# Performance work log

Measured on AMD Instinct MI355X. Metric: run time of the kernel, lower is better.

Reference implementation:

```python
import jax, jax.numpy as jnp
import numpy as np

H = 2048  # hidden_dim


def setup_inputs() -> dict:
    key = jax.random.key(0)
    ks = jax.random.split(key, 7)
    s = 1.0 / np.sqrt(H)
    x = jax.random.normal(ks[0], (4, 2048, H), dtype=jnp.float32)
    Wq = jax.random.uniform(ks[1], (H, H), jnp.float32, -s, s)
    Wk = jax.random.uniform(ks[2], (H, H), jnp.float32, -s, s)
    Wv = jax.random.uniform(ks[3], (H, H), jnp.float32, -s, s)
    Wo = jax.random.uniform(ks[4], (H, H), jnp.float32, -s, s)
    W1 = jax.random.uniform(ks[5], (H, H), jnp.float32, -s, s)
    W2 = jax.random.uniform(ks[6], (H, H), jnp.float32, -s, s)
    return {"x": x, "Wq": Wq, "Wk": Wk, "Wv": Wv, "Wo": Wo, "W1": W1, "W2": W2}


def reference(x, Wq, Wk, Wv, Wo, W1, W2):
    # Attention (single head, no 1/sqrt(d) scaling, no mask "" faithful to source)
    q = jnp.einsum('bsh,dh->bsd', x, Wq)
    k = jnp.einsum('bsh,dh->bsd', x, Wk)
    v = jnp.einsum('bsh,dh->bsd', x, Wv)
    score = jax.nn.softmax(jnp.einsum('bqd,bkd->bqk', q, k), axis=-1)
    attn = jnp.einsum('bqk,bkd->bqd', score, v)
    attn = jnp.einsum('bsh,dh->bsd', attn, Wo)
    # FFN
    h = jax.nn.relu(jnp.einsum('bsh,dh->bsd', attn, W1))
    y = jnp.einsum('bsh,dh->bsd', h, W2)
    return jnp.sum(y)
```

## Files before the change

kernel.cpp:

```cpp
#include <hip/hip_runtime.h>
#include <hip/hip_bf16.h>
#include <stdint.h>

typedef _Float16 h16_t;
typedef __attribute__((ext_vector_type(8))) _Float16 h16x8;
typedef __attribute__((ext_vector_type(4))) _Float16 h16x4;
typedef __attribute__((ext_vector_type(16))) float f32x16;

static constexpr int HDIM  = 2048;
static constexpr int MROWS = 8192;

__device__ __forceinline__ void gload_lds16(const h16_t* g, h16_t* l) {
  __builtin_amdgcn_global_load_lds(
      (const __attribute__((address_space(1))) void*)g,
      (__attribute__((address_space(3))) void*)l, 16, 0, 0);
}

__device__ __forceinline__ uint32_t ldsaddr(const void* p) {
  return (uint32_t)(uintptr_t)(const __attribute__((address_space(3))) void*)p;
}

__device__ __forceinline__ h16x8 dsread(uint32_t off) {
  h16x8 r;
  asm volatile("ds_read_b128 %0, %1" : "=v"(r) : "v"(off));
  return r;
}

__device__ __forceinline__ void sbar()  { __builtin_amdgcn_sched_barrier(0); }
__device__ __forceinline__ void bar()   { sbar(); __builtin_amdgcn_s_barrier(); sbar(); }
__device__ __forceinline__ void waitlg0(){ asm volatile("s_waitcnt lgkmcnt(0)" ::: "memory"); sbar(); }
__device__ __forceinline__ void waitvm4(){ asm volatile("s_waitcnt vmcnt(4)" ::: "memory"); sbar(); }
__device__ __forceinline__ void waitvm0(){ asm volatile("s_waitcnt vmcnt(0)" ::: "memory"); sbar(); }

__device__ __forceinline__ void gemm_core(const h16_t* __restrict__ A,
                                          const h16_t* __restrict__ B,
                                          f32x16 acc[2][2],
                                          h16_t* sA, h16_t* sB) {
  const int tid  = threadIdx.x;
  const int wid  = tid >> 6;
  const int lane = tid & 63;
  const int wr  = (wid >> 1) << 6;
  const int wc  = (wid & 1) << 6;
  const int l31 = lane & 31;
  const int hi  = lane >> 5;
  const int sx  = lane & 7;

#pragma unroll
  for (int i = 0; i < 2; i++)
#pragma unroll
    for (int j = 0; j < 2; j++)
#pragma unroll
      for (int r = 0; r < 16; r++) acc[i][j][r] = 0.0f;

  for (int k0 = 0; k0 < 2048; k0 += 64) {
    __syncthreads();
#pragma unroll
    for (int rnd = 0; rnd < 4; rnd++) {
      const int cid  = rnd * 256 + tid;
      const int row  = cid >> 3;
      const int koct = (cid & 7) ^ (row & 7);
      const long long goff = (long long)row * 2048 + k0 + koct * 8;
      gload_lds16(A + goff, sA + (rnd * 256 + wid * 64) * 8);
      gload_lds16(B + goff, sB + (rnd * 256 + wid * 64) * 8);
    }
    __syncthreads();

#pragma unroll
    for (int ko = 0; ko < 4; ko++) {
      const int po = (2 * ko + hi) ^ sx;
      h16x8 fa[2], fb[2];
#pragma unroll
      for (int i = 0; i < 2; i++)
        fa[i] = *(const h16x8*)(sA + (wr + i * 32 + l31) * 64 + po * 8);
#pragma unroll
      for (int j = 0; j < 2; j++)
        fb[j] = *(const h16x8*)(sB + (wc + j * 32 + l31) * 64 + po * 8);
#pragma unroll
      for (int i = 0; i < 2; i++)
#pragma unroll
        for (int j = 0; j < 2; j++)
          acc[i][j] = __builtin_amdgcn_mfma_f32_32x32x16_f16(
              fa[i], fb[j], acc[i][j], 0, 0, 0);
    }
  }
}

__device__ __forceinline__ void store_c(h16_t* __restrict__ C,
                                        f32x16 acc[2][2], int bm, int bn) {
  const int tid  = threadIdx.x;
  const int wid  = tid >> 6;
  const int lane = tid & 63;
  const int wr = (wid >> 1) << 6, wc = (wid & 1) << 6;
  const int l31 = lane & 31, hi = lane >> 5;
  const int gr = bm * 128 + wr + 4 * hi;
  const int gc = bn * 128 + wc + l31;
#pragma unroll
  for (int i = 0; i < 2; i++)
#pragma unroll
    for (int r = 0; r < 16; r++) {
      const int row = gr + i * 32 + (r & 3) + 8 * (r >> 2);
      const long long ro = (long long)row * 2048;
#pragma unroll
      for (int j = 0; j < 2; j++)
        C[ro + gc + j * 32] = (h16_t)acc[i][j][r];
    }
}

__global__ __launch_bounds__(256)
void gemm_b(const h16_t* __restrict__ Ab, const h16_t* __restrict__ Bb,
            h16_t* __restrict__ Cb, long long sAz, long long sBz, long long sCz)
{
  __shared__ __align__(16) h16_t sA[128 * 64];
  __shared__ __align__(16) h16_t sB[128 * 64];
  const int bn = blockIdx.x, bm = blockIdx.y, z = blockIdx.z;
  const h16_t* A = Ab + (long long)z * sAz + (long long)bm * 128 * 2048;
  const h16_t* B = Bb + (long long)z * sBz + (long long)bn * 128 * 2048;
  f32x16 acc[2][2];
  gemm_core(A, B, acc, sA, sB);
  store_c(Cb + (long long)z * sCz, acc, bm, bn);
}

__device__ __forceinline__ void core256(const h16_t* __restrict__ A,
                                        const h16_t* __restrict__ B,
                                        h16_t* smem, f32x16 acc[4][2])
{
  const int tid  = threadIdx.x;
  const int wid  = tid >> 6, lane = tid & 63;
  const int wr2  = wid >> 2, wcid = wid & 3;
  const int l31  = lane & 31, hi = lane >> 5, sx = lane & 7;

  h16_t* pA[2] = { smem,          smem + 32768 };
  h16_t* pB[2] = { smem + 16384,  smem + 49152 };

  uint32_t poB[4];
#pragma unroll
  for (int ks = 0; ks < 4; ks++) poB[ks] = (uint32_t)((((2 * ks + hi) ^ sx) << 4));
  const uint32_t lrow = (uint32_t)(l31 * 128);
  const uint32_t aT0 = ldsaddr(pA[0]) + (uint32_t)(wr2 * 16384) + lrow;
  const uint32_t aT1 = ldsaddr(pA[1]) + (uint32_t)(wr2 * 16384) + lrow;
  const uint32_t bT0 = ldsaddr(pB[0]) + (uint32_t)(wcid * 8192) + lrow;
  const uint32_t bT1 = ldsaddr(pB[1]) + (uint32_t)(wcid * 8192) + lrow;

  const int srow = tid >> 3;
  const long long stOff = (long long)srow * HDIM + (long long)(((tid & 7) ^ (srow & 7)) * 8);
  const int dOff = tid * 8;

  auto stage1 = [&](const h16_t* M, h16_t* panel, int k0, int ci) {
    gload_lds16(M + stOff + k0 + (long long)ci * (64 * HDIM),
                panel + ci * 4096 + dOff);
  };

#pragma unroll
  for (int i = 0; i < 4; i++)
#pragma unroll
    for (int j = 0; j < 2; j++)
#pragma unroll
      for (int r = 0; r < 16; r++) acc[i][j][r] = 0.0f;

  h16x8 fA[2][4], fB0[4], fB1[4];

  auto rdA = [&](uint32_t base) {
#pragma unroll
    for (int mi = 0; mi < 2; mi++)
#pragma unroll
      for (int ks = 0; ks < 4; ks++)
        fA[mi][ks] = dsread(base + (uint32_t)(mi * 4096) + poB[ks]);
  };
  auto rdB = [&](h16x8 (&fb)[4], uint32_t base) {
#pragma unroll
    for (int ks = 0; ks < 4; ks++) fb[ks] = dsread(base + poB[ks]);
  };
  auto mm8 = [&](int am0, int nj, h16x8 (&fb)[4]) {
#pragma unroll
    for (int ks = 0; ks < 4; ks++)
#pragma unroll
      for (int mi = 0; mi < 2; mi++)
        acc[am0 + mi][nj] = __builtin_amdgcn_mfma_f32_32x32x16_f16(
            fA[mi][ks], fb[ks], acc[am0 + mi][nj], 0, 0, 0);
  };

  auto tile4 = [&](uint32_t aT, uint32_t bT, h16_t* pAcur,
                   h16_t* stB, int kB, bool doB,
                   int kA, bool doA, int tailmode) {
    rdA(aT);
    rdB(fB0, bT);
    if (doB) { stage1(B, stB, kB, 0); stage1(B, stB, kB, 1); }
    bar(); waitlg0();
    __builtin_amdgcn_s_setprio(1); mm8(0, 0, fB0); __builtin_amdgcn_s_setprio(0);
    bar();
    rdB(fB1, bT + 4096);
    if (doB) { stage1(B, stB, kB, 2); stage1(B, stB, kB, 3); }
    bar(); waitlg0();
    __builtin_amdgcn_s_setprio(1); mm8(0, 1, fB1); __builtin_amdgcn_s_setprio(0);
    bar();
    rdA(aT + 8192);
    if (doA) { stage1(A, pAcur, kA, 0); stage1(A, pAcur, kA, 2); }
    bar(); waitlg0();
    __builtin_amdgcn_s_setprio(1); mm8(2, 1, fB1); __builtin_amdgcn_s_setprio(0);
    bar();
    if (doA) { stage1(A, pAcur, kA, 1); stage1(A, pAcur, kA, 3); }
    bar();
    __builtin_amdgcn_s_setprio(1); mm8(2, 0, fB0); __builtin_amdgcn_s_setprio(0);
    if (tailmode == 0) waitvm4(); else if (tailmode == 1) waitvm0();
    bar();
  };

  stage1(A, pA[0], 0, 0); stage1(A, pA[0], 0, 1);
  stage1(A, pA[0], 0, 2); stage1(A, pA[0], 0, 3);
  stage1(B, pB[0], 0, 0); stage1(B, pB[0], 0, 1);
  stage1(B, pB[0], 0, 2); stage1(B, pB[0], 0, 3);
  stage1(A, pA[1], 64, 0); stage1(A, pA[1], 64, 1);
  stage1(A, pA[1], 64, 2); stage1(A, pA[1], 64, 3);
  waitvm4(); bar();

#pragma unroll 1
  for (int t = 0; t < 30; t += 2) {
    tile4(aT0, bT0, pA[0], pB[1], (t + 1) * 64, true, (t + 2) * 64, true, 0);
    tile4(aT1, bT1, pA[1], pB[0], (t + 2) * 64, true, (t + 3) * 64, true, 0);
  }
  tile4(aT0, bT0, pA[0], pB[1], 31 * 64, true, 0, false, 1);
  tile4(aT1, bT1, pA[1], nullptr, 0, false, 0, false, 2);
}

__device__ __forceinline__ void store256(h16_t* __restrict__ C,
                                         f32x16 acc[4][2], int bm, int bn)
{
  const int tid = threadIdx.x, wid = tid >> 6, lane = tid & 63;
  const int wr2 = wid >> 2, wcid = wid & 3;
  const int l31 = lane & 31, hi = lane >> 5;
  const int gr0 = bm * 256 + wr2 * 128 + 4 * hi;
  const int gc0 = bn * 256 + wcid * 64 + l31;
#pragma unroll
  for (int am = 0; am < 4; am++)
#pragma unroll
    for (int r = 0; r < 16; r++) {
      const int row = gr0 + am * 32 + (r & 3) + 8 * (r >> 2);
      const long long ro = (long long)row * HDIM;
#pragma unroll
      for (int nj = 0; nj < 2; nj++)
        C[ro + gc0 + nj * 32] = (h16_t)acc[am][nj][r];
    }
}

template<int GY>
__device__ __forceinline__ void remap256(int& bn, int& bm, int& z) {
  const int flat = blockIdx.x + 8 * (blockIdx.y + GY * blockIdx.z);
  const int l = (flat & 7) * 32 + (flat >> 3);
  bn = l & 7;
  const int rest = l >> 3;
  bm = rest & (GY - 1);
  z  = rest / GY;
}

template<int GY>
__global__ __launch_bounds__(512, 2)
void gemm256_b(const h16_t* __restrict__ Ab, const h16_t* __restrict__ Bb,
               h16_t* __restrict__ Cb, long long sAz, long long sBz, long long sCz)
{
  __shared__ __align__(16) h16_t smem[4 * 16384];
  int bn, bm, z;
  remap256<GY>(bn, bm, z);
  const h16_t* A = Ab + (long long)z * sAz + (long long)bm * 256 * HDIM;
  const h16_t* B = Bb + (long long)z * sBz + (long long)bn * 256 * HDIM;
  f32x16 acc[4][2];
  core256(A, B, smem, acc);
  store256(Cb + (long long)z * sCz, acc, bm, bn);
}

__global__ __launch_bounds__(512, 2)
void gemm256_ut_softmax(const h16_t* __restrict__ Wvow, const h16_t* __restrict__ xb,
                        h16_t* __restrict__ ut, h16_t* __restrict__ sc)
{
  const int tid = threadIdx.x;
  if (blockIdx.z >= 4) {
    const int wid = tid >> 6, lane = tid & 63;
    const long long row = (long long)(blockIdx.z - 4) * 512 +
                          (blockIdx.y * 8 + blockIdx.x) * 8 + wid;
    h16_t* s = sc + row * HDIM;
    h16x8 raw[4];
#pragma unroll
    for (int i = 0; i < 4; i++) raw[i] = ((const h16x8*)s)[i * 64 + lane];
    float v[32];
    float mx = -3.0e38f;
#pragma unroll
    for (int i = 0; i < 32; i++) { v[i] = (float)raw[i >> 3][i & 7]; mx = fmaxf(mx, v[i]); }
#pragma unroll
    for (int off = 32; off; off >>= 1) mx = fmaxf(mx, __shfl_xor(mx, off, 64));
    float sum = 0.f;
#pragma unroll
    for (int i = 0; i < 32; i++) { v[i] = __expf(v[i] - mx); sum += v[i]; }
#pragma unroll
    for (int off = 32; off; off >>= 1) sum += __shfl_xor(sum, off, 64);
    const float inv = 1.0f / sum;
#pragma unroll
    for (int i = 0; i < 4; i++) {
      h16x8 o;
#pragma unroll
      for (int j = 0; j < 8; j++) o[j] = (h16_t)(v[i * 8 + j] * inv);
      ((h16x8*)s)[i * 64 + lane] = o;
    }
    return;
  }
  __shared__ __align__(16) h16_t smem[4 * 16384];
  int bn, bm, z;
  remap256<8>(bn, bm, z);
  const h16_t* A = Wvow + (long long)bm * 256 * HDIM;
  const h16_t* B = xb + (long long)z * (long long)HDIM * HDIM + (long long)bn * 256 * HDIM;
  f32x16 acc[4][2];
  core256(A, B, smem, acc);
  store256(ut + (long long)z * (long long)HDIM * HDIM, acc, bm, bn);
}

__global__ __launch_bounds__(512, 2)
void gemm256_final(const h16_t* __restrict__ P, const h16_t* __restrict__ utb,
                   const float* __restrict__ w2p, float* __restrict__ outp)
{
  __shared__ __align__(16) h16_t smem[4 * 16384];
  int bn, bm, z;
  remap256<8>(bn, bm, z);
  const long long HH = (long long)HDIM * HDIM;
  const h16_t* A = P   + (long long)z * HH + (long long)bm * 256 * HDIM;
  const h16_t* B = utb + (long long)z * HH + (long long)bn * 256 * HDIM;
  f32x16 acc[4][2];
  core256(A, B, smem, acc);

  const int tid = threadIdx.x, wid = tid >> 6, lane = tid & 63;
  const int wcid = wid & 3, l31 = lane & 31;
  const int gc0 = bn * 256 + wcid * 64 + l31;
  float w2j[2];
#pragma unroll
  for (int nj = 0; nj < 2; nj++) {
    const int col = gc0 + nj * 32;
    float s = 0.f;
#pragma unroll
    for (int c = 0; c < 32; c++) s += w2p[c * HDIM + col];
    w2j[nj] = s;
  }
  float s = 0.f;
#pragma unroll
  for (int am = 0; am < 4; am++)
#pragma unroll
    for (int nj = 0; nj < 2; nj++)
#pragma unroll
      for (int r = 0; r < 16; r++) {
        const float vv = acc[am][nj][r];
        s += (vv > 0.f) ? vv * w2j[nj] : 0.f;
      }
#pragma unroll
  for (int off = 32; off; off >>= 1) s += __shfl_down(s, off, 64);
  __shared__ float red[8];
  if (lane == 0) red[wid] = s;
  __syncthreads();
  if (tid == 0) {
    float t = 0.f;
#pragma unroll
    for (int w = 0; w < 8; w++) t += red[w];
    atomicAdd(outp, t);
  }
}

__global__ __launch_bounds__(256)
void prologue_kernel(const float* __restrict__ x,  const float* __restrict__ Wq,
                     const float* __restrict__ Wk, const float* __restrict__ Wv,
                     const float* __restrict__ Wo, const float* __restrict__ W1,
                     const float* __restrict__ W2,
                     h16_t* __restrict__ xb,  h16_t* __restrict__ WkT,
                     h16_t* __restrict__ WvT, h16_t* __restrict__ WqT,
                     h16_t* __restrict__ Wob, h16_t* __restrict__ W1b,
                     float* __restrict__ w2p, float* __restrict__ outp)
{
  const int t = threadIdx.x;
  int b = blockIdx.x;
  if (b < 16384) {
    const long long i = (long long)b * 256 + t;
    const float4 v = ((const float4*)x)[i];
    h16x4 o;
    o[0] = (h16_t)v.x; o[1] = (h16_t)v.y; o[2] = (h16_t)v.z; o[3] = (h16_t)v.w;
    ((h16x4*)xb)[i] = o;
    return;
  }
  b -= 16384;
  if (b < 3072) {
    const float* src; h16_t* dst;
    const int w = b >> 10, b10 = b & 1023;
    if (w == 0)      { src = Wk; dst = WkT; }
    else if (w == 1) { src = Wv; dst = WvT; }
    else             { src = Wq; dst = WqT; }
    __shared__ float tl[64][65];
    const int bx = (b10 & 31) * 64, by = (b10 >> 5) * 64;
#pragma unroll
    for (int i = 0; i < 4; i++) {
      const int idx = i * 256 + t;
      const int r = idx >> 4, c4 = idx & 15;
      const float4 v = *(const float4*)(src + (long long)(by + r) * 2048 + bx + c4 * 4);
      tl[r][c4 * 4 + 0] = v.x; tl[r][c4 * 4 + 1] = v.y;
      tl[r][c4 * 4 + 2] = v.z; tl[r][c4 * 4 + 3] = v.w;
    }
    __syncthreads();
#pragma unroll
    for (int i = 0; i < 2; i++) {
      const int idx = i * 256 + t;
      const int c = idx >> 3, r8 = (idx & 7) * 8;
      h16x8 o;
#pragma unroll
      for (int j = 0; j < 8; j++) o[j] = (h16_t)tl[r8 + j][c];
      *(h16x8*)(dst + (long long)(bx + c) * 2048 + by + r8) = o;
    }
    return;
  }
  b -= 3072;
  if (b < 8192) {
    const float* src = (b < 4096) ? Wo : W1;
    h16_t* dst = (b < 4096) ? Wob : W1b;
    const long long i = (long long)(b & 4095) * 256 + t;
    const float4 v = ((const float4*)src)[i];
    h16x4 o;
    o[0] = (h16_t)v.x; o[1] = (h16_t)v.y; o[2] = (h16_t)v.z; o[3] = (h16_t)v.w;
    ((h16x4*)dst)[i] = o;
    return;
  }
  b -= 8192;
  if (b < 256) {
    const int c = b >> 3;
    const int h = (b & 7) * 256 + t;
    float s = 0.f;
#pragma unroll 4
    for (int d = 0; d < 64; d++) s += W2[(long long)(c * 64 + d) * 2048 + h];
    w2p[c * 2048 + h] = s;
    return;
  }
  b -= 256;
  if (b == 0 && t == 0) outp[0] = 0.f;
}

extern "C" void kernel_launch(void* const* d_in, const int* in_sizes, int n_in,
                              void* d_out, int out_size, void* d_ws, size_t ws_size,
                              hipStream_t stream)
{
  const float* x  = (const float*)d_in[0];
  const float* Wq = (const float*)d_in[1];
  const float* Wk = (const float*)d_in[2];
  const float* Wv = (const float*)d_in[3];
  const float* Wo = (const float*)d_in[4];
  const float* W1 = (const float*)d_in[5];
  const float* W2 = (const float*)d_in[6];
  float* out = (float*)d_out;

  const long long HH = (long long)HDIM * HDIM;
  const long long XE = (long long)MROWS * HDIM;

  char* p = (char*)d_ws;
  h16_t* xb   = (h16_t*)p; p += XE * 2;
  h16_t* WkT  = (h16_t*)p; p += HH * 2;
  h16_t* WvT  = (h16_t*)p; p += HH * 2;
  h16_t* WqT  = (h16_t*)p; p += HH * 2;
  h16_t* Wob  = (h16_t*)p; p += HH * 2;
  h16_t* WqkT = (h16_t*)p; p += HH * 2;
  h16_t* GT   = (h16_t*)p; p += HH * 2;
  h16_t* W1b  = (h16_t*)p; p += HH * 2;
  h16_t* Wvow = (h16_t*)p; p += HH * 2;
  h16_t* tb   = (h16_t*)p; p += XE * 2;
  h16_t* sc   = (h16_t*)p; p += XE * 2;
  float* w2p  = (float*)p; p += 32 * HDIM * 4;

  const dim3 b256(256), b512(512);

  prologue_kernel<<<dim3(16384 + 3072 + 8192 + 256 + 1), b256, 0, stream>>>(
      x, Wq, Wk, Wv, Wo, W1, W2, xb, WkT, WvT, WqT, Wob, W1b, w2p, out);

  gemm_b<<<dim3(16, 16, 2), b256, 0, stream>>>(WkT, WqT, WqkT, HH, HH, HH);

  gemm_b<<<dim3(16, 16, 1), b256, 0, stream>>>(W1b, GT, Wvow, 0, 0, 0);

  gemm256_b<32><<<dim3(8, 32, 1), b512, 0, stream>>>(xb, WqkT, tb, 0, 0, 0);

  gemm256_b<8><<<dim3(8, 8, 4), b512, 0, stream>>>(tb, xb, sc, HH, HH, HH);

  gemm256_ut_softmax<<<dim3(8, 8, 20), b512, 0, stream>>>(Wvow, xb, tb, sc);

  gemm256_final<<<dim3(8, 8, 4), b512, 0, stream>>>(sc, tb, w2p, out);
}
```

Baseline: 532.4 us.

## Split fused ut-GEMM/softmax kernel, relax sched barriers, use single-block launch bounds

Splits the combined ut-GEMM plus softmax launch into a standalone softmax kernel followed by a plain gemm256_b launch for the ut product. It removes most sched_barrier fences around s_barrier and vmcnt waits, which gives the compiler more freedom to interleave instructions. It also changes launch bounds from 2 to 1 blocks per CU so the GEMMs get more registers. The trade-offs are an extra kernel launch, no overlap between softmax and the GEMM, and possible reordering hazards from the removed fences.

```diff
diff --git a/kernel.cpp b/kernel.cpp
--- a/kernel.cpp
+++ b/kernel.cpp
@@ -26,11 +26,11 @@
   return r;
 }
 
-__device__ __forceinline__ void sbar()  { __builtin_amdgcn_sched_barrier(0); }
-__device__ __forceinline__ void bar()   { sbar(); __builtin_amdgcn_s_barrier(); sbar(); }
-__device__ __forceinline__ void waitlg0(){ asm volatile("s_waitcnt lgkmcnt(0)" ::: "memory"); sbar(); }
-__device__ __forceinline__ void waitvm4(){ asm volatile("s_waitcnt vmcnt(4)" ::: "memory"); sbar(); }
-__device__ __forceinline__ void waitvm0(){ asm volatile("s_waitcnt vmcnt(0)" ::: "memory"); sbar(); }
+__device__ __forceinline__ void bar()    { __builtin_amdgcn_s_barrier(); }
+__device__ __forceinline__ void waitlg0(){ asm volatile("s_waitcnt lgkmcnt(0)" ::: "memory");
+                                           __builtin_amdgcn_sched_barrier(0); }
+__device__ __forceinline__ void waitvm4(){ asm volatile("s_waitcnt vmcnt(4)" ::: "memory"); }
+__device__ __forceinline__ void waitvm0(){ asm volatile("s_waitcnt vmcnt(0)" ::: "memory"); }
 
 __device__ __forceinline__ void gemm_core(const h16_t* __restrict__ A,
                                           const h16_t* __restrict__ B,
@@ -253,7 +253,7 @@
 }
 
 template<int GY>
-__global__ __launch_bounds__(512, 2)
+__global__ __launch_bounds__(512, 1)
 void gemm256_b(const h16_t* __restrict__ Ab, const h16_t* __restrict__ Bb,
                h16_t* __restrict__ Cb, long long sAz, long long sBz, long long sCz)
 {
@@ -267,51 +267,37 @@
   store256(Cb + (long long)z * sCz, acc, bm, bn);
 }
 
-__global__ __launch_bounds__(512, 2)
-void gemm256_ut_softmax(const h16_t* __restrict__ Wvow, const h16_t* __restrict__ xb,
-                        h16_t* __restrict__ ut, h16_t* __restrict__ sc)
-{
-  const int tid = threadIdx.x;
-  if (blockIdx.z >= 4) {
-    const int wid = tid >> 6, lane = tid & 63;
-    const long long row = (long long)(blockIdx.z - 4) * 512 +
-                          (blockIdx.y * 8 + blockIdx.x) * 8 + wid;
-    h16_t* s = sc + row * HDIM;
-    h16x8 raw[4];
-#pragma unroll
-    for (int i = 0; i < 4; i++) raw[i] = ((const h16x8*)s)[i * 64 + lane];
-    float v[32];
-    float mx = -3.0e38f;
-#pragma unroll
-    for (int i = 0; i < 32; i++) { v[i] = (float)raw[i >> 3][i & 7]; mx = fmaxf(mx, v[i]); }
-#pragma unroll
-    for (int off = 32; off; off >>= 1) mx = fmaxf(mx, __shfl_xor(mx, off, 64));
-    float sum = 0.f;
-#pragma unroll
-    for (int i = 0; i < 32; i++) { v[i] = __expf(v[i] - mx); sum += v[i]; }
-#pragma unroll
-    for (int off = 32; off; off >>= 1) sum += __shfl_xor(sum, off, 64);
-    const float inv = 1.0f / sum;
-#pragma unroll
-    for (int i = 0; i < 4; i++) {
-      h16x8 o;
-#pragma unroll
-      for (int j = 0; j < 8; j++) o[j] = (h16_t)(v[i * 8 + j] * inv);
-      ((h16x8*)s)[i * 64 + lane] = o;
-    }
-    return;
-  }
-  __shared__ __align__(16) h16_t smem[4 * 16384];
-  int bn, bm, z;
-  remap256<8>(bn, bm, z);
-  const h16_t* A = Wvow + (long long)bm * 256 * HDIM;
-  const h16_t* B = xb + (long long)z * (long long)HDIM * HDIM + (long long)bn * 256 * HDIM;
-  f32x16 acc[4][2];
-  core256(A, B, smem, acc);
-  store256(ut + (long long)z * (long long)HDIM * HDIM, acc, bm, bn);
-}
-
-__global__ __launch_bounds__(512, 2)
+__global__ __launch_bounds__(512)
+void softmax_kernel(h16_t* __restrict__ sc)
+{
+  const int tid = threadIdx.x, wid = tid >> 6, lane = tid & 63;
+  const long long row = (long long)blockIdx.x * 8 + wid;
+  h16_t* s = sc + row * HDIM;
+  h16x8 raw[4];
+#pragma unroll
+  for (int i = 0; i < 4; i++) raw[i] = ((const h16x8*)s)[i * 64 + lane];
+  float v[32];
+  float mx = -3.0e38f;
+#pragma unroll
+  for (int i = 0; i < 32; i++) { v[i] = (float)raw[i >> 3][i & 7]; mx = fmaxf(mx, v[i]); }
+#pragma unroll
+  for (int off = 32; off; off >>= 1) mx = fmaxf(mx, __shfl_xor(mx, off, 64));
+  float sum = 0.f;
+#pragma unroll
+  for (int i = 0; i < 32; i++) { v[i] = __expf(v[i] - mx); sum += v[i]; }
+#pragma unroll
+  for (int off = 32; off; off >>= 1) sum += __shfl_xor(sum, off, 64);
+  const float inv = 1.0f / sum;
+#pragma unroll
+  for (int i = 0; i < 4; i++) {
+    h16x8 o;
+#pragma unroll
+    for (int j = 0; j < 8; j++) o[j] = (h16_t)(v[i * 8 + j] * inv);
+    ((h16x8*)s)[i * 64 + lane] = o;
+  }
+}
+
+__global__ __launch_bounds__(512, 1)
 void gemm256_final(const h16_t* __restrict__ P, const h16_t* __restrict__ utb,
                    const float* __restrict__ w2p, float* __restrict__ outp)
 {
@@ -476,7 +462,9 @@
 
   gemm256_b<8><<<dim3(8, 8, 4), b512, 0, stream>>>(tb, xb, sc, HH, HH, HH);
 
-  gemm256_ut_softmax<<<dim3(8, 8, 20), b512, 0, stream>>>(Wvow, xb, tb, sc);
+  softmax_kernel<<<dim3(1024), b512, 0, stream>>>(sc);
+
+  gemm256_b<8><<<dim3(8, 8, 4), b512, 0, stream>>>(Wvow, xb, tb, 0, HH, HH);
 
   gemm256_final<<<dim3(8, 8, 4), b512, 0, stream>>>(sc, tb, w2p, out);
 }
```

New measurement: 527.1 us. No clear change (-1.0%).
